# Optimization experiments

Measured on AMD Instinct MI355X. Metric: run time of the kernel, lower is better.

Reference implementation:

```python
import math
import jax, jax.numpy as jnp
import numpy as np

C = 1.0          # Poincare ball curvature
NUM_HEADS = 8
EPS = 1e-15

def _beta(a, b):
    # Beta function via lgamma (python float constant)
    return math.exp(math.lgamma(a) + math.lgamma(b) - math.lgamma(a + b))

def h_linear(x, z, r, c=C):
    """HNN++ Poincare fully-connected layer (hypll HLinear).
    x: [..., in] points in the ball; z: [in, out] tangent weights; r: [out] bias."""
    sc = math.sqrt(c)
    x2 = jnp.sum(x * x, axis=-1, keepdims=True)
    lam = 2.0 / (1.0 - c * x2)                                # conformal factor
    zn = jnp.maximum(jnp.linalg.norm(z, axis=0), EPS)          # [out]
    inner = x @ z                                              # [..., out]
    two_scr = 2.0 * sc * r
    d = (2.0 * zn / sc) * jnp.arcsinh(
        (sc * inner * lam / zn) * jnp.cosh(two_scr) - (lam - 1.0) * jnp.sinh(two_scr)
    )
    w = jnp.sinh(sc * d) / sc
    return w / (1.0 + jnp.sqrt(1.0 + c * jnp.sum(w * w, axis=-1, keepdims=True)))

def pairwise_dist(q, k, c=C):
    """Poincare distance d(q,k) = arccosh(1 + 2c|q-k|^2 / ((1-c|q|^2)(1-c|k|^2))) / sqrt(c).
    q,k: [B,H,S,hd] -> [B,H,S,S]."""
    q2 = jnp.sum(q * q, axis=-1)
    k2 = jnp.sum(k * k, axis=-1)
    qk = jnp.einsum('bhqd,bhkd->bhqk', q, k)
    diff2 = jnp.maximum(q2[..., :, None] + k2[..., None, :] - 2.0 * qk, 0.0)
    denom = (1.0 - c * q2)[..., :, None] * (1.0 - c * k2)[..., None, :]
    arg = 1.0 + 2.0 * c * diff2 / denom
    return jnp.arccosh(jnp.maximum(arg, 1.0 + 1e-7)) / math.sqrt(c)

def midpoint(v, w, c=C):
    """Weighted Mobius gyromidpoint: m = 1/2 (x) (sum w*lam*x / sum w*(lam-1)).
    v: [B,H,Sk,hd], w: [B,H,Sq,Sk] -> [B,H,Sq,hd]."""
    v2 = jnp.sum(v * v, axis=-1)                      # [B,H,Sk]
    lam = 2.0 / (1.0 - c * v2)
    num = jnp.einsum('bhqk,bhkd->bhqd', w * lam[..., None, :], v)
    den = jnp.maximum(jnp.einsum('bhqk,bhk->bhq', w, lam - 1.0), EPS)[..., None]
    g = num / den                                     # gyromidpoint pre-scaling
    sc = math.sqrt(c)
    gn = jnp.maximum(jnp.linalg.norm(g, axis=-1, keepdims=True), EPS)
    t = jnp.tanh(0.5 * jnp.arctanh(jnp.clip(sc * gn, 0.0, 1.0 - 1e-7)))
    return (t / sc) * g / gn

def _forward(query, key, value, Wq, bq, Wk, bk, Wv, bv, scale_tau, scale_gamma):
    B, S, E = query.shape
    H = NUM_HEADS
    hd = E // H
    # hyperbolic q/k/v projections, then split into heads: [B,H,S,hd]
    q = h_linear(query, Wq, bq).reshape(B, S, H, hd).transpose(0, 2, 1, 3)
    k = h_linear(key, Wk, bk).reshape(B, S, H, hd).transpose(0, 2, 1, 3)
    v = h_linear(value, Wv, bv).reshape(B, S, H, hd).transpose(0, 2, 1, 3)
    # similarity = -dist/tau - gamma with tau = exp(-scale_tau)
    sim = -pairwise_dist(q, k) * jnp.exp(scale_tau[0]) - scale_gamma[0]
    causal = jnp.triu(jnp.ones((S, S), dtype=bool), k=1)
    sim = jnp.where(causal, -jnp.inf, sim)
    w = jnp.exp(sim)                                  # 'exp' attention activation
    agg = midpoint(v, w)                              # [B,H,S,hd]
    agg = agg.transpose(0, 2, 1, 3).reshape(B, S, E)
    # HNN++ beta-concatenation of the per-head ball points
    scale = _beta(E / 2.0, 0.5) / _beta(hd / 2.0, 0.5)
    return agg * scale

def setup_inputs() -> dict:
    root = jax.random.key(0)
    ks = jax.random.split(root, 8)
    B, S, E = 1, 2048, 512
    s = 0.02  # keep points well inside the unit ball
    return {
        'query': s * jax.random.normal(ks[0], (B, S, E), jnp.float32),
        'key':   s * jax.random.normal(ks[1], (B, S, E), jnp.float32),
        'value': s * jax.random.normal(ks[2], (B, S, E), jnp.float32),
        'Wq': s * jax.random.normal(ks[3], (E, E), jnp.float32),
        'Wk': s * jax.random.normal(ks[4], (E, E), jnp.float32),
        'Wv': s * jax.random.normal(ks[5], (E, E), jnp.float32),
        'bq': jnp.zeros((E,), jnp.float32),
        'bk': jnp.zeros((E,), jnp.float32),
        'bv': jnp.zeros((E,), jnp.float32),
        'scale_tau': jnp.zeros((1,), jnp.float32),
        'scale_gamma': jnp.zeros((1,), jnp.float32),
    }

def reference(query, key, value, Wq, Wk, Wv, bq, bk, bv, scale_tau, scale_gamma):
    return _forward(query, key, value, Wq, bq, Wk, bk, Wv, bv, scale_tau, scale_gamma)
```

## Files before the change

kernel.cpp:

```cpp
#include <hip/hip_runtime.h>
#include <cmath>

#define H 8
#define SEQ 2048
#define EDIM 512
#define HD 64
#define EPSF 1e-15f

typedef short bf16x8 __attribute__((ext_vector_type(8)));
typedef float f32x4 __attribute__((ext_vector_type(4)));

#define ZN_OFF    16
#define STATS_OFF (ZN_OFF + 24 * EDIM)
#define CQ_OFF    (STATS_OFF + 3 * H * SEQ)
#define IK_OFF    (CQ_OFF + H * SEQ)
#define PX2_OFF   (IK_OFF + H * SEQ)
#define U16_OFF   (PX2_OFF + 12288 + 16)
#define WT_U16    0
#define QKVB_U16  (WT_U16 + 3 * EDIM * EDIM)
#define VT_U16    (QKVB_U16 + 3 * SEQ * EDIM)
#define U16_TOTAL (VT_U16 + H * 80 * SEQ)
#define BIG_OFF   (U16_OFF + U16_TOTAL / 2 + 16)
#define PART_U16S (8 * 32 * 8 * 4 * 1280)
#define ACC_FLOATS  (H * SEQ * 80)

__device__ __forceinline__ float bf2f(unsigned short u){
  union { unsigned int i; float f; } v; v.i = ((unsigned int)u) << 16; return v.f;
}
__device__ __forceinline__ unsigned short f2bf(float f){
  union { float f; unsigned int i; } v; v.f = f;
  unsigned int x = v.i;
  unsigned int r = (x + 0x7fffu + ((x >> 16) & 1u)) >> 16;
  return (unsigned short)r;
}

__device__ __forceinline__ int detect_f32(const unsigned short* __restrict__ q){
  const int l = threadIdx.x & 63;
  float mx = 0.f;
  #pragma unroll
  for (int j = 0; j < 4; ++j) mx = fmaxf(mx, fabsf(bf2f(q[l * 4 + j])));
  #pragma unroll
  for (int m = 32; m >= 1; m >>= 1) mx = fmaxf(mx, __shfl_xor(mx, m, 64));
  return mx > 1000.f;
}

__global__ __launch_bounds__(256) void wcvt_kernel(
    const void* __restrict__ Wq, const void* __restrict__ Wk, const void* __restrict__ Wv,
    const unsigned short* __restrict__ qprobe,
    unsigned short* __restrict__ WT, float* __restrict__ zn)
{
  const int p = blockIdx.y;
  const int bi = blockIdx.x >> 3, bo = blockIdx.x & 7;
  const void* W = (p == 0) ? Wq : ((p == 1) ? Wk : Wv);
  const int t = threadIdx.x;
  const int isf32 = detect_f32(qprobe);
  __shared__ float tile[64][65];

  #pragma unroll
  for (int j = 0; j < 16; ++j){
    int idx = t + 256 * j;
    int il = idx >> 6, ol = idx & 63;
    float val;
    if (isf32) val = ((const float*)W)[(size_t)(bi * 64 + il) * EDIM + bo * 64 + ol];
    else       val = bf2f(((const unsigned short*)W)[(size_t)(bi * 64 + il) * EDIM + bo * 64 + ol]);
    tile[il][ol] = val;
  }
  __syncthreads();
  if (t < 64){
    float s = 0.f;
    #pragma unroll 8
    for (int i = 0; i < 64; ++i){ float v = tile[i][t]; s += v * v; }
    zn[((size_t)(bi * 3 + p)) * EDIM + bo * 64 + t] = s;
  }
  #pragma unroll
  for (int j = 0; j < 16; ++j){
    int idx = t + 256 * j;
    int ol = idx >> 6, il = idx & 63;
    WT[((size_t)p * EDIM + bo * 64 + ol) * EDIM + bi * 64 + il] = f2bf(tile[il][ol]);
  }
}

__global__ __launch_bounds__(256) void hlin_gemm_kernel(
    const void* __restrict__ Xq, const void* __restrict__ Xk, const void* __restrict__ Xv,
    const unsigned short* __restrict__ WT, const unsigned short* __restrict__ qprobe,
    unsigned short* __restrict__ partC, float* __restrict__ partX2)
{
  const int p = blockIdx.y;
  const int rg = blockIdx.x >> 1;
  const int kslice = blockIdx.x & 1;
  const void* X = (p == 0) ? Xq : ((p == 1) ? Xk : Xv);
  const int r0 = rg * 16;
  const int t  = threadIdx.x;
  const int w = t >> 6, lane = t & 63;
  const int col = lane & 15, quad = lane >> 4;
  const int isf32 = detect_f32(qprobe);
  const int koff = kslice * 256;

  const unsigned short* WTb = WT + ((size_t)p * EDIM + w * 128 + col) * EDIM + koff;
  const float* Xf = (const float*)X + (size_t)(r0 + col) * EDIM + koff;
  const unsigned short* Xh = (const unsigned short*)X + (size_t)(r0 + col) * EDIM + koff;

  f32x4 acc[8];
  #pragma unroll
  for (int nt = 0; nt < 8; ++nt) acc[nt] = (f32x4){0.f, 0.f, 0.f, 0.f};
  float x2part = 0.f;

  bf16x8 caf, naf;
  bf16x8 cbf[8], nbf[8];
  {
    if (isf32){
      float4 xa = *(const float4*)&Xf[quad * 8];
      float4 xb = *(const float4*)&Xf[quad * 8 + 4];
      float xv[8] = {xa.x, xa.y, xa.z, xa.w, xb.x, xb.y, xb.z, xb.w};
      #pragma unroll
      for (int j = 0; j < 8; ++j){ caf[j] = (short)f2bf(xv[j]); x2part += xv[j] * xv[j]; }
    } else {
      caf = *(const bf16x8*)&Xh[quad * 8];
      #pragma unroll
      for (int j = 0; j < 8; ++j){ float xv = bf2f((unsigned short)caf[j]); x2part += xv * xv; }
    }
    #pragma unroll
    for (int nt = 0; nt < 8; ++nt)
      cbf[nt] = *(const bf16x8*)&WTb[(size_t)nt * 16 * EDIM + quad * 8];
  }

  for (int ks = 0; ks < 8; ++ks){
    if (ks + 1 < 8){
      const int off = (ks + 1) * 32 + quad * 8;
      if (isf32){
        float4 xa = *(const float4*)&Xf[off];
        float4 xb = *(const float4*)&Xf[off + 4];
        float xv[8] = {xa.x, xa.y, xa.z, xa.w, xb.x, xb.y, xb.z, xb.w};
        #pragma unroll
        for (int j = 0; j < 8; ++j){ naf[j] = (short)f2bf(xv[j]); x2part += xv[j] * xv[j]; }
      } else {
        naf = *(const bf16x8*)&Xh[off];
        #pragma unroll
        for (int j = 0; j < 8; ++j){ float xv = bf2f((unsigned short)naf[j]); x2part += xv * xv; }
      }
      #pragma unroll
      for (int nt = 0; nt < 8; ++nt)
        nbf[nt] = *(const bf16x8*)&WTb[(size_t)nt * 16 * EDIM + off];
    }
    #pragma unroll
    for (int nt = 0; nt < 8; ++nt)
      acc[nt] = __builtin_amdgcn_mfma_f32_16x16x32_bf16(caf, cbf[nt], acc[nt], 0, 0, 0);
    if (ks + 1 < 8){
      caf = naf;
      #pragma unroll
      for (int nt = 0; nt < 8; ++nt) cbf[nt] = nbf[nt];
    }
  }
  x2part += __shfl_xor(x2part, 16, 64);
  x2part += __shfl_xor(x2part, 32, 64);

  const size_t base = ((size_t)(p * 128 + rg) * 2 + kslice) * 8192;
  #pragma unroll
  for (int nt = 0; nt < 8; ++nt)
    #pragma unroll
    for (int r = 0; r < 4; ++r)
      partC[base + (size_t)(quad * 4 + r) * 512 + w * 128 + nt * 16 + col] = f2bf(acc[nt][r]);
  if (w == 0 && quad == 0)
    partX2[((size_t)(p * 128 + rg) * 2 + kslice) * 16 + col] = x2part;
}

__global__ __launch_bounds__(256) void hlin_fin_kernel(
    const unsigned short* __restrict__ partC, const float* __restrict__ partX2,
    const void* __restrict__ Bq, const void* __restrict__ Bk, const void* __restrict__ Bv,
    const float* __restrict__ znacc, const unsigned short* __restrict__ qprobe,
    unsigned short* __restrict__ qkvb, float* __restrict__ stats,
    float* __restrict__ cqs, float* __restrict__ iks,
    unsigned short* __restrict__ VT)
{
  const int p = blockIdx.y;
  const void* Bb = (p == 0) ? Bq : ((p == 1) ? Bk : Bv);
  const int rg = blockIdx.x;
  const int r0 = rg * 16;
  const int t  = threadIdx.x;
  const int w = t >> 6, lane = t & 63;
  const int col = lane & 15, quad = lane >> 4;
  const int isf32 = detect_f32(qprobe);

  __shared__ float smem[16 * EDIM];
  __shared__ float sw2[16];

  const size_t base0 = ((size_t)(p * 128 + rg) * 2 + 0) * 8192;
  const size_t base1 = base0 + 8192;

  f32x4 acc[8];
  #pragma unroll
  for (int nt = 0; nt < 8; ++nt)
    #pragma unroll
    for (int r = 0; r < 4; ++r){
      const size_t idx = (size_t)(quad * 4 + r) * 512 + w * 128 + nt * 16 + col;
      acc[nt][r] = bf2f(partC[base0 + idx]) + bf2f(partC[base1 + idx]);
    }

  float lamr[4], lm1[4];
  #pragma unroll
  for (int r = 0; r < 4; ++r){
    const int row = quad * 4 + r;
    float x2r = partX2[((size_t)(p * 128 + rg) * 2 + 0) * 16 + row] +
                partX2[((size_t)(p * 128 + rg) * 2 + 1) * 16 + row];
    lamr[r] = 2.f / (1.f - x2r);
    lm1[r] = lamr[r] - 1.f;
  }
  #pragma unroll
  for (int nt = 0; nt < 8; ++nt){
    const int n = w * 128 + nt * 16 + col;
    float zsum = 0.f;
    #pragma unroll
    for (int bi = 0; bi < 8; ++bi)
      zsum += znacc[((size_t)(bi * 3 + p)) * EDIM + n];
    float znv = fmaxf(sqrtf(zsum), EPSF);
    float rb;
    if (isf32) rb = ((const float*)Bb)[n];
    else       rb = bf2f(((const unsigned short*)Bb)[n]);
    float e2r = __expf(2.f * rb);
    float ie2r = 1.f / e2r;
    float ch = 0.5f * (e2r + ie2r), sh = 0.5f * (e2r - ie2r);
    float izn = 1.f / znv;
    float tz = 2.f * znv;
    #pragma unroll
    for (int r = 0; r < 4; ++r){
      float a = (acc[nt][r] * lamr[r] * izn) * ch - lm1[r] * sh;
      float b = a + sqrtf(a * a + 1.f);
      float tt = __expf(tz * __logf(b));
      smem[(quad * 4 + r) * EDIM + n] = 0.5f * (tt - 1.f / tt);
    }
  }
  __syncthreads();

  {
    int row = t >> 4, l = t & 15;
    float s = 0.f;
    for (int o = l; o < EDIM; o += 16){ float wv = smem[row * EDIM + o]; s += wv * wv; }
    #pragma unroll
    for (int m = 8; m >= 1; m >>= 1) s += __shfl_xor(s, m, 16);
    if (l == 0) sw2[row] = s;
  }
  __syncthreads();

  const int o0 = 2 * t;
  const int h0 = t >> 5;
  const int d0 = o0 & 63;
  const int l5 = t & 31;
  #pragma unroll
  for (int rr = 0; rr < 16; ++rr){
    float inv = 1.f / (1.f + sqrtf(1.f + sw2[rr]));
    unsigned short b0 = f2bf(smem[rr * EDIM + o0] * inv);
    unsigned short b1 = f2bf(smem[rr * EDIM + o0 + 1] * inv);
    float r0v = bf2f(b0), r1v = bf2f(b1);
    int s = r0 + rr;
    unsigned int* dst = (unsigned int*)&qkvb[(((size_t)p * H + h0) * SEQ + s) * HD + d0];
    *dst = (unsigned int)b0 | ((unsigned int)b1 << 16);
    float ss = r0v * r0v + r1v * r1v;
    #pragma unroll
    for (int m = 16; m >= 1; m >>= 1) ss += __shfl_xor(ss, m, 64);
    if (p == 2){
      float lam = 2.f / (1.f - ss);
      VT[((size_t)h0 * 80 + d0) * SEQ + s]     = f2bf(r0v * lam);
      VT[((size_t)h0 * 80 + d0 + 1) * SEQ + s] = f2bf(r1v * lam);
      if (l5 < 16)
        VT[((size_t)h0 * 80 + 64 + l5) * SEQ + s] = (l5 == 0) ? f2bf(lam - 1.f) : 0;
    }
    if (l5 == 0){
      stats[((size_t)p * H + h0) * SEQ + s] = ss;
      if (p == 0) cqs[(size_t)h0 * SEQ + s] = 2.f / (1.f - ss);
      if (p == 1) iks[(size_t)h0 * SEQ + s] = 1.f / (1.f - ss);
    }
  }
}

__global__ __launch_bounds__(64) void attn_kernel(
    const unsigned short* __restrict__ Qb, const unsigned short* __restrict__ Kb,
    const unsigned short* __restrict__ VT,
    const float* __restrict__ q2s_all, const float* __restrict__ k2s_all,
    const float* __restrict__ cqs_all, const float* __restrict__ iks_all,
    const void* __restrict__ tau, const void* __restrict__ gam,
    const unsigned short* __restrict__ qprobe,
    float* __restrict__ big, int use_part)
{
  const int h  = blockIdx.y;
  const int tile = 31 - (blockIdx.x >> 5);
  const int sl = (blockIdx.x >> 2) & 7;
  const int w  = blockIdx.x & 3;
  if (sl > tile) return;
  const int lane = threadIdx.x;
  const int col = lane & 15, quad = lane >> 4;
  const int q0 = tile * 64 + w * 16;

  const unsigned short* Qh  = Qb + (size_t)h * SEQ * HD;
  const unsigned short* Kh  = Kb + (size_t)h * SEQ * HD;
  const unsigned short* VTh = VT + (size_t)h * 80 * SEQ;
  const float* q2s = q2s_all + (size_t)h * SEQ;
  const float* k2s = k2s_all + (size_t)h * SEQ;
  const float* cqs = cqs_all + (size_t)h * SEQ;
  const float* iks = iks_all + (size_t)h * SEQ;

  const int isf32 = detect_f32(qprobe);
  float tauv, gamv;
  if (isf32){ tauv = ((const float*)tau)[0]; gamv = ((const float*)gam)[0]; }
  else      { tauv = bf2f(((const unsigned short*)tau)[0]);
              gamv = bf2f(((const unsigned short*)gam)[0]); }
  const float e_tau = __expf(tauv);

  const int srcA = ((quad & 1) * 2) * 16 + col;
  const int srcB = srcA + 16;
  const int tsel = quad >> 1;

  bf16x8 qf0 = *(const bf16x8*)&Qh[(size_t)(q0 + col) * HD + quad * 8];
  bf16x8 qf1 = *(const bf16x8*)&Qh[(size_t)(q0 + col) * HD + 32 + quad * 8];
  const float q2 = q2s[q0 + col];
  const float cq = cqs[q0 + col];
  const int qmax = q0 + col;

  f32x4 pv[5];
  #pragma unroll
  for (int nt = 0; nt < 5; ++nt) pv[nt] = (f32x4){0.f, 0.f, 0.f, 0.f};

  const int nch = ((tile - sl) >> 3) + 1;
  const int nhalf = nch * 2;
  int kb32 = sl * 64;

  bf16x8 ckf0[2], ckf1[2], nkf0[2], nkf1[2];
  float4 ck2[2], cik[2], nk2[2], nik[2];
  #pragma unroll
  for (int tt = 0; tt < 2; ++tt){
    const int kbase = kb32 + 16 * tt;
    ckf0[tt] = *(const bf16x8*)&Kh[(size_t)(kbase + col) * HD + quad * 8];
    ckf1[tt] = *(const bf16x8*)&Kh[(size_t)(kbase + col) * HD + 32 + quad * 8];
    ck2[tt]  = *(const float4*)&k2s[kbase + quad * 4];
    cik[tt]  = *(const float4*)&iks[kbase + quad * 4];
  }

  for (int i = 0; i < nhalf; ++i){
    const int nkb32 = (i & 1) ? (kb32 + 512 - 32) : (kb32 + 32);
    const bool have_next = (i + 1 < nhalf);
    if (have_next){
      #pragma unroll
      for (int tt = 0; tt < 2; ++tt){
        const int kbase = nkb32 + 16 * tt;
        nkf0[tt] = *(const bf16x8*)&Kh[(size_t)(kbase + col) * HD + quad * 8];
        nkf1[tt] = *(const bf16x8*)&Kh[(size_t)(kbase + col) * HD + 32 + quad * 8];
        nk2[tt]  = *(const float4*)&k2s[kbase + quad * 4];
        nik[tt]  = *(const float4*)&iks[kbase + quad * 4];
      }
    }

    unsigned int tlo[2], thi[2];
    #pragma unroll
    for (int tt = 0; tt < 2; ++tt){
      const int kbase = kb32 + 16 * tt;
      f32x4 s = (f32x4){0.f, 0.f, 0.f, 0.f};
      s = __builtin_amdgcn_mfma_f32_16x16x32_bf16(ckf0[tt], qf0, s, 0, 0, 0);
      s = __builtin_amdgcn_mfma_f32_16x16x32_bf16(ckf1[tt], qf1, s, 0, 0, 0);
      unsigned short pb[4];
      #pragma unroll
      for (int r = 0; r < 4; ++r){
        float k2 = (r == 0) ? ck2[tt].x : (r == 1) ? ck2[tt].y : (r == 2) ? ck2[tt].z : ck2[tt].w;
        float ik = (r == 0) ? cik[tt].x : (r == 1) ? cik[tt].y : (r == 2) ? cik[tt].z : cik[tt].w;
        float diff2 = fmaxf(q2 + k2 - 2.f * s[r], 0.f);
        float u = fmaxf(diff2 * cq * ik, 1e-7f);
        float z = 1.f + u + sqrtf(u * (u + 2.f));
        float dist = __logf(z);
        float wv = __expf(-e_tau * dist - gamv);
        int key = kbase + quad * 4 + r;
        if (key > qmax) wv = 0.f;
        pb[r] = f2bf(wv);
      }
      tlo[tt] = (unsigned int)pb[0] | ((unsigned int)pb[1] << 16);
      thi[tt] = (unsigned int)pb[2] | ((unsigned int)pb[3] << 16);
    }
    unsigned int a0 = (unsigned int)__shfl((int)tlo[0], srcA, 64);
    unsigned int a1 = (unsigned int)__shfl((int)tlo[1], srcA, 64);
    unsigned int b0 = (unsigned int)__shfl((int)thi[0], srcA, 64);
    unsigned int b1 = (unsigned int)__shfl((int)thi[1], srcA, 64);
    unsigned int c0 = (unsigned int)__shfl((int)tlo[0], srcB, 64);
    unsigned int c1 = (unsigned int)__shfl((int)tlo[1], srcB, 64);
    unsigned int d0 = (unsigned int)__shfl((int)thi[0], srcB, 64);
    unsigned int d1 = (unsigned int)__shfl((int)thi[1], srcB, 64);
    union { uint4 u; bf16x8 v; } pw;
    pw.u.x = tsel ? a1 : a0;
    pw.u.y = tsel ? b1 : b0;
    pw.u.z = tsel ? c1 : c0;
    pw.u.w = tsel ? d1 : d0;
    #pragma unroll
    for (int nt = 0; nt < 5; ++nt){
      bf16x8 vf = *(const bf16x8*)&VTh[(size_t)(16 * nt + col) * SEQ + kb32 + quad * 8];
      pv[nt] = __builtin_amdgcn_mfma_f32_16x16x32_bf16(pw.v, vf, pv[nt], 0, 0, 0);
    }

    if (have_next){
      #pragma unroll
      for (int tt = 0; tt < 2; ++tt){
        ckf0[tt] = nkf0[tt]; ckf1[tt] = nkf1[tt];
        ck2[tt] = nk2[tt];   cik[tt] = nik[tt];
      }
    }
    kb32 = nkb32;
  }

  if (use_part){
    uint2* slot = (uint2*)big + (size_t)((((h * 32 + tile) * 8) + sl) * 4 + w) * 320;
    #pragma unroll
    for (int nt = 0; nt < 5; ++nt){
      uint2 pk;
      pk.x = (unsigned int)f2bf(pv[nt][0]) | ((unsigned int)f2bf(pv[nt][1]) << 16);
      pk.y = (unsigned int)f2bf(pv[nt][2]) | ((unsigned int)f2bf(pv[nt][3]) << 16);
      slot[nt * 64 + lane] = pk;
    }
  } else {
    #pragma unroll
    for (int r = 0; r < 4; ++r){
      float* row = big + ((size_t)h * SEQ + q0 + quad * 4 + r) * 80;
      #pragma unroll
      for (int nt = 0; nt < 5; ++nt)
        atomicAdd(&row[16 * nt + col], pv[nt][r]);
    }
  }
}

__global__ __launch_bounds__(256) void attn_fin_kernel(
    const float* __restrict__ big, int use_part,
    float* __restrict__ out, float beta_scale)
{
  const int h = blockIdx.y, tile16 = blockIdx.x;
  const int t = threadIdx.x;
  const int w = t >> 6, lane = t & 63;
  const int col = lane & 15, quad = lane >> 4;
  const int q0 = tile16 * 16;

  __shared__ float red[4][64][20];

  f32x4 pv[5];
  #pragma unroll
  for (int nt = 0; nt < 5; ++nt) pv[nt] = (f32x4){0.f, 0.f, 0.f, 0.f};

  if (use_part){
    const int st = tile16 >> 2, wq = tile16 & 3;
    const int nv = (st + 1 < 8) ? st + 1 : 8;
    for (int sl = w; sl < nv; sl += 4){
      const uint2* slot = (const uint2*)big +
          (size_t)((((h * 32 + st) * 8) + sl) * 4 + wq) * 320;
      #pragma unroll
      for (int nt = 0; nt < 5; ++nt){
        uint2 v = slot[nt * 64 + lane];
        pv[nt][0] += bf2f((unsigned short)(v.x & 0xffffu));
        pv[nt][1] += bf2f((unsigned short)(v.x >> 16));
        pv[nt][2] += bf2f((unsigned short)(v.y & 0xffffu));
        pv[nt][3] += bf2f((unsigned short)(v.y >> 16));
      }
    }
  } else if (w == 0){
    #pragma unroll
    for (int nt = 0; nt < 5; ++nt)
      #pragma unroll
      for (int r = 0; r < 4; ++r)
        pv[nt][r] = big[((size_t)h * SEQ + q0 + quad * 4 + r) * 80 + 16 * nt + col];
  }

  #pragma unroll
  for (int nt = 0; nt < 5; ++nt)
    *(float4*)&red[w][lane][nt * 4] = (float4){pv[nt][0], pv[nt][1], pv[nt][2], pv[nt][3]};
  __syncthreads();

  if (t < 64){
    #pragma unroll
    for (int nt = 0; nt < 5; ++nt){
      float4 a = *(const float4*)&red[0][t][nt * 4];
      float4 b = *(const float4*)&red[1][t][nt * 4];
      float4 c = *(const float4*)&red[2][t][nt * 4];
      float4 d = *(const float4*)&red[3][t][nt * 4];
      pv[nt][0] = a.x + b.x + c.x + d.x;
      pv[nt][1] = a.y + b.y + c.y + d.y;
      pv[nt][2] = a.z + b.z + c.z + d.z;
      pv[nt][3] = a.w + b.w + c.w + d.w;
    }
    #pragma unroll
    for (int r = 0; r < 4; ++r){
      float den = __shfl(pv[4][r], quad * 16, 64);
      den = fmaxf(den, EPSF);
      float inv_den = 1.f / den;
      float g[4];
      float gsq = 0.f;
      #pragma unroll
      for (int nt = 0; nt < 4; ++nt){ g[nt] = pv[nt][r] * inv_den; gsq += g[nt] * g[nt]; }
      #pragma unroll
      for (int m = 8; m >= 1; m >>= 1) gsq += __shfl_xor(gsq, m, 64);
      float gn = fmaxf(sqrtf(gsq), EPSF);
      float x = fminf(gn, 1.f - 1e-7f);
      float tt2 = x / (1.f + sqrtf(1.f - x * x));
      float scl = (tt2 / gn) * beta_scale;
      const int q = q0 + quad * 4 + r;
      #pragma unroll
      for (int nt = 0; nt < 4; ++nt)
        out[(size_t)q * EDIM + h * HD + 16 * nt + col] = g[nt] * scl;
    }
  }
}

extern "C" void kernel_launch(void* const* d_in, const int* in_sizes, int n_in,
                              void* d_out, int out_size, void* d_ws, size_t ws_size,
                              hipStream_t stream){
  const void* Xq  = d_in[0];
  const void* Xk  = d_in[1];
  const void* Xv  = d_in[2];
  const void* Wq  = d_in[3];
  const void* Wk  = d_in[4];
  const void* Wv  = d_in[5];
  const void* Bq  = d_in[6];
  const void* Bk  = d_in[7];
  const void* Bv  = d_in[8];
  const void* tau = d_in[9];
  const void* gam = d_in[10];

  float* wsf   = (float*)d_ws;
  float* zn    = wsf + ZN_OFF;
  float* stats = wsf + STATS_OFF;
  float* cqs   = wsf + CQ_OFF;
  float* iks   = wsf + IK_OFF;
  float* px2   = wsf + PX2_OFF;
  unsigned short* u16b = (unsigned short*)(wsf + U16_OFF);
  unsigned short* WT   = u16b + WT_U16;
  unsigned short* qkvb = u16b + QKVB_U16;
  unsigned short* VT   = u16b + VT_U16;
  float* big   = wsf + BIG_OFF;
  unsigned short* partC = (unsigned short*)big;

  const int use_part =
      (ws_size >= (size_t)BIG_OFF * sizeof(float) + (size_t)PART_U16S * 2) ? 1 : 0;

  unsigned short* Qb = qkvb;
  unsigned short* Kb = qkvb + (size_t)H * SEQ * HD;
  float* q2s = stats;
  float* k2s = stats + (size_t)H * SEQ;
  const unsigned short* qprobe = (const unsigned short*)Xq;

  double lb1 = lgamma(EDIM / 2.0) + lgamma(0.5) - lgamma(EDIM / 2.0 + 0.5);
  double lb2 = lgamma(HD / 2.0)   + lgamma(0.5) - lgamma(HD / 2.0 + 0.5);
  float beta_scale = (float)exp(lb1 - lb2);

  wcvt_kernel<<<dim3(64, 3), dim3(256), 0, stream>>>(Wq, Wk, Wv, qprobe, WT, zn);
  hlin_gemm_kernel<<<dim3(256, 3), dim3(256), 0, stream>>>(
      Xq, Xk, Xv, WT, qprobe, partC, px2);
  hlin_fin_kernel<<<dim3(128, 3), dim3(256), 0, stream>>>(
      partC, px2, Bq, Bk, Bv, zn, qprobe, qkvb, stats, cqs, iks, VT);
  if (!use_part)
    hipMemsetAsync(big, 0, (size_t)ACC_FLOATS * sizeof(float), stream);
  attn_kernel<<<dim3(32 * 8 * 4, H), dim3(64), 0, stream>>>(
      Qb, Kb, VT, q2s, k2s, cqs, iks, tau, gam, qprobe, big, use_part);
  attn_fin_kernel<<<dim3(128, H), dim3(256), 0, stream>>>(
      big, use_part, (float*)d_out, beta_scale);
}
```

Before: 203.1 us.

## Process two query sub-tiles per wavefront to reuse K and V fragments

Each attention wavefront now handles two 16-row query blocks, rows wp*16 and wp*16+32 within the 64-row tile, instead of one. The same K and V fragments loaded from global memory feed MFMAs for both blocks, which halves the grid size and the K/V load traffic per query row. In exchange each wave uses roughly twice the accumulator and Q registers, which may lower occupancy, and there are half as many waves to hide latency.

```diff
diff --git a/kernel.cpp b/kernel.cpp
--- a/kernel.cpp
+++ b/kernel.cpp
@@ -282,13 +282,14 @@
     float* __restrict__ big, int use_part)
 {
   const int h  = blockIdx.y;
-  const int tile = 31 - (blockIdx.x >> 5);
-  const int sl = (blockIdx.x >> 2) & 7;
-  const int w  = blockIdx.x & 3;
+  const int tile = 31 - (blockIdx.x >> 4);
+  const int sl = (blockIdx.x >> 1) & 7;
+  const int wp = blockIdx.x & 1;
   if (sl > tile) return;
   const int lane = threadIdx.x;
   const int col = lane & 15, quad = lane >> 4;
-  const int q0 = tile * 64 + w * 16;
+  const int q0A = tile * 64 + wp * 16;
+  const int q0B = q0A + 32;
 
   const unsigned short* Qh  = Qb + (size_t)h * SEQ * HD;
   const unsigned short* Kh  = Kb + (size_t)h * SEQ * HD;
@@ -309,15 +310,20 @@
   const int srcB = srcA + 16;
   const int tsel = quad >> 1;
 
-  bf16x8 qf0 = *(const bf16x8*)&Qh[(size_t)(q0 + col) * HD + quad * 8];
-  bf16x8 qf1 = *(const bf16x8*)&Qh[(size_t)(q0 + col) * HD + 32 + quad * 8];
-  const float q2 = q2s[q0 + col];
-  const float cq = cqs[q0 + col];
-  const int qmax = q0 + col;
-
-  f32x4 pv[5];
-  #pragma unroll
-  for (int nt = 0; nt < 5; ++nt) pv[nt] = (f32x4){0.f, 0.f, 0.f, 0.f};
+  bf16x8 qfA0 = *(const bf16x8*)&Qh[(size_t)(q0A + col) * HD + quad * 8];
+  bf16x8 qfA1 = *(const bf16x8*)&Qh[(size_t)(q0A + col) * HD + 32 + quad * 8];
+  bf16x8 qfB0 = *(const bf16x8*)&Qh[(size_t)(q0B + col) * HD + quad * 8];
+  bf16x8 qfB1 = *(const bf16x8*)&Qh[(size_t)(q0B + col) * HD + 32 + quad * 8];
+  const float q2A = q2s[q0A + col], q2B = q2s[q0B + col];
+  const float cqA = cqs[q0A + col], cqB = cqs[q0B + col];
+  const int qmaxA = q0A + col, qmaxB = q0B + col;
+
+  f32x4 pvA[5], pvB[5];
+  #pragma unroll
+  for (int nt = 0; nt < 5; ++nt){
+    pvA[nt] = (f32x4){0.f, 0.f, 0.f, 0.f};
+    pvB[nt] = (f32x4){0.f, 0.f, 0.f, 0.f};
+  }
 
   const int nch = ((tile - sl) >> 3) + 1;
   const int nhalf = nch * 2;
@@ -348,47 +354,78 @@
       }
     }
 
-    unsigned int tlo[2], thi[2];
+    unsigned int tloA[2], thiA[2], tloB[2], thiB[2];
     #pragma unroll
     for (int tt = 0; tt < 2; ++tt){
       const int kbase = kb32 + 16 * tt;
-      f32x4 s = (f32x4){0.f, 0.f, 0.f, 0.f};
-      s = __builtin_amdgcn_mfma_f32_16x16x32_bf16(ckf0[tt], qf0, s, 0, 0, 0);
-      s = __builtin_amdgcn_mfma_f32_16x16x32_bf16(ckf1[tt], qf1, s, 0, 0, 0);
-      unsigned short pb[4];
+      f32x4 sA = (f32x4){0.f, 0.f, 0.f, 0.f};
+      f32x4 sB = (f32x4){0.f, 0.f, 0.f, 0.f};
+      sA = __builtin_amdgcn_mfma_f32_16x16x32_bf16(ckf0[tt], qfA0, sA, 0, 0, 0);
+      sB = __builtin_amdgcn_mfma_f32_16x16x32_bf16(ckf0[tt], qfB0, sB, 0, 0, 0);
+      sA = __builtin_amdgcn_mfma_f32_16x16x32_bf16(ckf1[tt], qfA1, sA, 0, 0, 0);
+      sB = __builtin_amdgcn_mfma_f32_16x16x32_bf16(ckf1[tt], qfB1, sB, 0, 0, 0);
+      unsigned short pbA[4], pbB[4];
       #pragma unroll
       for (int r = 0; r < 4; ++r){
         float k2 = (r == 0) ? ck2[tt].x : (r == 1) ? ck2[tt].y : (r == 2) ? ck2[tt].z : ck2[tt].w;
         float ik = (r == 0) ? cik[tt].x : (r == 1) ? cik[tt].y : (r == 2) ? cik[tt].z : cik[tt].w;
-        float diff2 = fmaxf(q2 + k2 - 2.f * s[r], 0.f);
-        float u = fmaxf(diff2 * cq * ik, 1e-7f);
-        float z = 1.f + u + sqrtf(u * (u + 2.f));
-        float dist = __logf(z);
-        float wv = __expf(-e_tau * dist - gamv);
-        int key = kbase + quad * 4 + r;
-        if (key > qmax) wv = 0.f;
-        pb[r] = f2bf(wv);
+        const int key = kbase + quad * 4 + r;
+        {
+          float diff2 = fmaxf(q2A + k2 - 2.f * sA[r], 0.f);
+          float u = fmaxf(diff2 * cqA * ik, 1e-7f);
+          float z = 1.f + u + sqrtf(u * (u + 2.f));
+          float wv = __expf(-e_tau * __logf(z) - gamv);
+          if (key > qmaxA) wv = 0.f;
+          pbA[r] = f2bf(wv);
+        }
+        {
+          float diff2 = fmaxf(q2B + k2 - 2.f * sB[r], 0.f);
+          float u = fmaxf(diff2 * cqB * ik, 1e-7f);
+          float z = 1.f + u + sqrtf(u * (u + 2.f));
+          float wv = __expf(-e_tau * __logf(z) - gamv);
+          if (key > qmaxB) wv = 0.f;
+          pbB[r] = f2bf(wv);
+        }
       }
-      tlo[tt] = (unsigned int)pb[0] | ((unsigned int)pb[1] << 16);
-      thi[tt] = (unsigned int)pb[2] | ((unsigned int)pb[3] << 16);
-    }
-    unsigned int a0 = (unsigned int)__shfl((int)tlo[0], srcA, 64);
-    unsigned int a1 = (unsigned int)__shfl((int)tlo[1], srcA, 64);
-    unsigned int b0 = (unsigned int)__shfl((int)thi[0], srcA, 64);
-    unsigned int b1 = (unsigned int)__shfl((int)thi[1], srcA, 64);
-    unsigned int c0 = (unsigned int)__shfl((int)tlo[0], srcB, 64);
-    unsigned int c1 = (unsigned int)__shfl((int)tlo[1], srcB, 64);
-    unsigned int d0 = (unsigned int)__shfl((int)thi[0], srcB, 64);
-    unsigned int d1 = (unsigned int)__shfl((int)thi[1], srcB, 64);
-    union { uint4 u; bf16x8 v; } pw;
-    pw.u.x = tsel ? a1 : a0;
-    pw.u.y = tsel ? b1 : b0;
-    pw.u.z = tsel ? c1 : c0;
-    pw.u.w = tsel ? d1 : d0;
+      tloA[tt] = (unsigned int)pbA[0] | ((unsigned int)pbA[1] << 16);
+      thiA[tt] = (unsigned int)pbA[2] | ((unsigned int)pbA[3] << 16);
+      tloB[tt] = (unsigned int)pbB[0] | ((unsigned int)pbB[1] << 16);
+      thiB[tt] = (unsigned int)pbB[2] | ((unsigned int)pbB[3] << 16);
+    }
+    union { uint4 u; bf16x8 v; } pwA, pwB;
+    {
+      unsigned int a0 = (unsigned int)__shfl((int)tloA[0], srcA, 64);
+      unsigned int a1 = (unsigned int)__shfl((int)tloA[1], srcA, 64);
+      unsigned int b0 = (unsigned int)__shfl((int)thiA[0], srcA, 64);
+      unsigned int b1 = (unsigned int)__shfl((int)thiA[1], srcA, 64);
+      unsigned int c0 = (unsigned int)__shfl((int)tloA[0], srcB, 64);
+      unsigned int c1 = (unsigned int)__shfl((int)tloA[1], srcB, 64);
+      unsigned int d0 = (unsigned int)__shfl((int)thiA[0], srcB, 64);
+      unsigned int d1 = (unsigned int)__shfl((int)thiA[1], srcB, 64);
+      pwA.u.x = tsel ? a1 : a0;
+      pwA.u.y = tsel ? b1 : b0;
+      pwA.u.z = tsel ? c1 : c0;
+      pwA.u.w = tsel ? d1 : d0;
+    }
+    {
+      unsigned int a0 = (unsigned int)__shfl((int)tloB[0], srcA, 64);
+      unsigned int a1 = (unsigned int)__shfl((int)tloB[1], srcA, 64);
+      unsigned int b0 = (unsigned int)__shfl((int)thiB[0], srcA, 64);
+      unsigned int b1 = (unsigned int)__shfl((int)thiB[1], srcA, 64);
+      unsigned int c0 = (unsigned int)__shfl((int)tloB[0], srcB, 64);
+      unsigned int c1 = (unsigned int)__shfl((int)tloB[1], srcB, 64);
+      unsigned int d0 = (unsigned int)__shfl((int)thiB[0], srcB, 64);
+      unsigned int d1 = (unsigned int)__shfl((int)thiB[1], srcB, 64);
+      pwB.u.x = tsel ? a1 : a0;
+      pwB.u.y = tsel ? b1 : b0;
+      pwB.u.z = tsel ? c1 : c0;
+      pwB.u.w = tsel ? d1 : d0;
+    }
     #pragma unroll
     for (int nt = 0; nt < 5; ++nt){
       bf16x8 vf = *(const bf16x8*)&VTh[(size_t)(16 * nt + col) * SEQ + kb32 + quad * 8];
-      pv[nt] = __builtin_amdgcn_mfma_f32_16x16x32_bf16(pw.v, vf, pv[nt], 0, 0, 0);
+      pvA[nt] = __builtin_amdgcn_mfma_f32_16x16x32_bf16(pwA.v, vf, pvA[nt], 0, 0, 0);
+      pvB[nt] = __builtin_amdgcn_mfma_f32_16x16x32_bf16(pwB.v, vf, pvB[nt], 0, 0, 0);
     }
 
     if (have_next){
@@ -402,21 +439,28 @@
   }
 
   if (use_part){
-    uint2* slot = (uint2*)big + (size_t)((((h * 32 + tile) * 8) + sl) * 4 + w) * 320;
+    uint2* slotA = (uint2*)big + (size_t)((((h * 32 + tile) * 8) + sl) * 4 + wp) * 320;
+    uint2* slotB = (uint2*)big + (size_t)((((h * 32 + tile) * 8) + sl) * 4 + wp + 2) * 320;
     #pragma unroll
     for (int nt = 0; nt < 5; ++nt){
       uint2 pk;
-      pk.x = (unsigned int)f2bf(pv[nt][0]) | ((unsigned int)f2bf(pv[nt][1]) << 16);
-      pk.y = (unsigned int)f2bf(pv[nt][2]) | ((unsigned int)f2bf(pv[nt][3]) << 16);
-      slot[nt * 64 + lane] = pk;
+      pk.x = (unsigned int)f2bf(pvA[nt][0]) | ((unsigned int)f2bf(pvA[nt][1]) << 16);
+      pk.y = (unsigned int)f2bf(pvA[nt][2]) | ((unsigned int)f2bf(pvA[nt][3]) << 16);
+      slotA[nt * 64 + lane] = pk;
+      pk.x = (unsigned int)f2bf(pvB[nt][0]) | ((unsigned int)f2bf(pvB[nt][1]) << 16);
+      pk.y = (unsigned int)f2bf(pvB[nt][2]) | ((unsigned int)f2bf(pvB[nt][3]) << 16);
+      slotB[nt * 64 + lane] = pk;
     }
   } else {
     #pragma unroll
     for (int r = 0; r < 4; ++r){
-      float* row = big + ((size_t)h * SEQ + q0 + quad * 4 + r) * 80;
-      #pragma unroll
-      for (int nt = 0; nt < 5; ++nt)
-        atomicAdd(&row[16 * nt + col], pv[nt][r]);
+      float* rowA = big + ((size_t)h * SEQ + q0A + quad * 4 + r) * 80;
+      float* rowB = big + ((size_t)h * SEQ + q0B + quad * 4 + r) * 80;
+      #pragma unroll
+      for (int nt = 0; nt < 5; ++nt){
+        atomicAdd(&rowA[16 * nt + col], pvA[nt][r]);
+        atomicAdd(&rowB[16 * nt + col], pvB[nt][r]);
+      }
     }
   }
 }
@@ -548,7 +592,7 @@
       partC, px2, Bq, Bk, Bv, zn, qprobe, qkvb, stats, cqs, iks, VT);
   if (!use_part)
     hipMemsetAsync(big, 0, (size_t)ACC_FLOATS * sizeof(float), stream);
-  attn_kernel<<<dim3(32 * 8 * 4, H), dim3(64), 0, stream>>>(
+  attn_kernel<<<dim3(32 * 8 * 2, H), dim3(64), 0, stream>>>(
       Qb, Kb, VT, q2s, k2s, cqs, iks, tau, gam, qprobe, big, use_part);
   attn_fin_kernel<<<dim3(128, H), dim3(256), 0, stream>>>(
       big, use_part, (float*)d_out, beta_scale);
```

Measured after the change: 201.0 us, median of 2. No clear change (-1.0%).
